# Kernel tuning notes

Hardware: AMD Instinct MI355X
Metric: run time of the kernel (lower is better)

The kernel has to match this reference:

```python
import jax, jax.numpy as jnp
import numpy as np

B, IC, H, W = 8, 16, 32, 32
OC, KH, KW = 32, 3, 3
PAD, K = 1, 2
OH, OW = H, W  # stride 1, pad 1, dilation 1 with 3x3 kernel
TABLES = OC * IC * KH * KW  # 4608, one LUT per (oc, ic, kh, kw)
M = TABLES * K              # 9216 mask rows
NUM_ENTRIES = 2 ** K


def setup_inputs() -> dict:
    key = jax.random.key(0)
    k1, k2, k3, k4, k5 = jax.random.split(key, 5)
    inp = jax.random.normal(k1, (B, IC, H, W), dtype=jnp.float32)
    w_luts = jax.random.normal(k2, (TABLES, NUM_ENTRIES), dtype=jnp.float32)
    mask_c = jax.random.randint(k3, (M,), 0, IC)
    mask_kh = jax.random.randint(k4, (M,), 0, KH)
    mask_kw = jax.random.randint(k5, (M,), 0, KW)
    return {"input": inp, "w_luts": w_luts, "mask_c": mask_c,
            "mask_kh": mask_kh, "mask_kw": mask_kw}


def _truth_table():
    # tt[j, i] in {-1, +1}: sign of bit j of truth-table entry i
    entries = jnp.arange(NUM_ENTRIES)
    bits = (entries[None, :] >> jnp.arange(K)[:, None]) & 1  # (K, 2^K)
    return (2 * bits - 1).astype(jnp.float32)


def reference(input, w_luts, mask_c, mask_kh, mask_kw):
    # Fused unfold (im2col) + per-table input_mask gather: instead of
    # materializing folded_input (B, L, IC, KH, KW), gather straight from the
    # padded image: expanded[b, oh, ow, m] = padded[b, c_m, oh + kh_m, ow + kw_m]
    padded = jnp.pad(input, ((0, 0), (0, 0), (PAD, PAD), (PAD, PAD)))
    row = jnp.arange(OH)[:, None] + mask_kh[None, :]   # (OH, M)
    col = jnp.arange(OW)[:, None] + mask_kw[None, :]   # (OW, M)
    expanded = padded[:, mask_c[None, None, :], row[:, None, :], col[None, :, :]]  # (B, OH, OW, M)

    # LagrangeTrainer: per-table soft LUT lookup via Lagrange interpolation
    x = expanded.reshape(B * OH * OW, TABLES, K)
    tt = _truth_table()                                       # (K, 2^K)
    factors = (1.0 + x[..., :, None] * tt[None, None]) * 0.5  # (N, T, K, 2^K)
    basis = jnp.prod(factors, axis=-2)                        # (N, T, 2^K)
    out = jnp.einsum('nte,te->nt', basis, w_luts)             # (N, TABLES)

    # Fold-style reshape + sum over the IC*KH*KW tables feeding each output
    out = out.reshape(B, OC, OH, OW, -1).sum(-1)
    out = out.reshape(B, OH * OW, OC).swapaxes(1, 2).reshape(B, OC, OH, OW)
    return out
```

## Files before the change

kernel.cpp:

```cpp
#include <hip/hip_runtime.h>

#define OC_ 32
#define IC_ 16
#define H_ 32
#define W_ 32
#define B_ 8
#define TPO 144

#define ROWS_PER_WG 16
#define TR 18
#define TC 34
#define CH_STRIDE (TR * TC)
#define TILE_F (IC_ * CH_STRIDE)

#define NQ 4
#define TQ (TPO / NQ)
#define NTHR 1024

struct alignas(16) Rec4 { unsigned offs; float bb, cc, dd; };

__global__ __launch_bounds__(NTHR, 8)
void conv_kernel(const float* __restrict__ input,
                 const float* __restrict__ w_luts,
                 const int*   __restrict__ mask_c,
                 const int*   __restrict__ mask_kh,
                 const int*   __restrict__ mask_kw,
                 float*       __restrict__ out) {
    __shared__ float tile[TILE_F];
    __shared__ Rec4  srec[TPO];
    __shared__ float sAA[TPO];
    __shared__ float sP[8];
    __shared__ float redA[NTHR];
    __shared__ float redB[NTHR];

    const int oh0 = blockIdx.x * ROWS_PER_WG;
    const int oc  = blockIdx.y;
    const int b   = blockIdx.z;
    const int tid = threadIdx.x;

    if (tid < TPO) {
        int t = oc * TPO + tid;
        const float4 w = *reinterpret_cast<const float4*>(w_luts + 4 * t);
        int m0 = 2 * t, m1 = m0 + 1;
        unsigned off0 = (unsigned)(mask_c[m0] * CH_STRIDE + mask_kh[m0] * TC + mask_kw[m0]) * 4u;
        unsigned off1 = (unsigned)(mask_c[m1] * CH_STRIDE + mask_kh[m1] * TC + mask_kw[m1]) * 4u;
        Rec4 r;
        r.offs = off0 | (off1 << 16);
        r.bb = 0.25f * (-w.x + w.y - w.z + w.w);
        r.cc = 0.25f * (-w.x - w.y + w.z + w.w);
        r.dd = 0.25f * ( w.x - w.y - w.z + w.w);
        srec[tid] = r;
        sAA[tid]  = 0.25f * (w.x + w.y + w.z + w.w);
    }

    const float* inb = input + b * (IC_ * H_ * W_);
    for (int u = tid; u < IC_ * TR * 8; u += NTHR) {
        int ch  = u / (TR * 8);
        int rem = u - ch * (TR * 8);
        int r   = rem >> 3;
        int c4  = (rem & 7) * 4;
        int grow = oh0 + r - 1;
        float4 v = make_float4(0.f, 0.f, 0.f, 0.f);
        if ((unsigned)grow < (unsigned)H_)
            v = *reinterpret_cast<const float4*>(inb + (ch * H_ + grow) * W_ + c4);
        float* dst = &tile[ch * CH_STRIDE + r * TC + 1 + c4];
        dst[0] = v.x; dst[1] = v.y; dst[2] = v.z; dst[3] = v.w;
    }
    for (int i = tid; i < IC_ * TR * 2; i += NTHR) {
        int ch  = i / (TR * 2);
        int rem = i - ch * (TR * 2);
        int r   = rem >> 1;
        int cc2 = (rem & 1) ? (TC - 1) : 0;
        tile[ch * CH_STRIDE + r * TC + cc2] = 0.f;
    }
    __syncthreads();

    if (tid < 8) {
        float s = 0.f;
        #pragma unroll
        for (int i = 0; i < 18; ++i) s += sAA[tid * 18 + i];
        sP[tid] = s;
    }

    const int pos = tid & 255;
    const int qt  = tid >> 8;
    const int rl  = pos >> 5;
    const int ow  = pos & 31;
    const char* tb = (const char*)tile + ((2 * rl) * TC + ow) * 4;
    const int4* sq = reinterpret_cast<const int4*>(srec);

    float accA = 0.f, accB = 0.f;
    const int t0 = qt * TQ;
    #pragma unroll 6
    for (int t = t0; t < t0 + TQ; ++t) {
        const int4 q = sq[t];
        const unsigned offs = (unsigned)q.x;
        const float* g0 = reinterpret_cast<const float*>(tb + (offs & 0xffffu));
        const float* g1 = reinterpret_cast<const float*>(tb + (offs >> 16));
        const float x0a = g0[0];
        const float x0b = g0[TC];
        const float x1a = g1[0];
        const float x1b = g1[TC];
        const float bb = __int_as_float(q.y);
        const float cc = __int_as_float(q.z);
        const float dd = __int_as_float(q.w);
        accA = fmaf(bb, x0a, accA);
        accA = fmaf(x1a, fmaf(dd, x0a, cc), accA);
        accB = fmaf(bb, x0b, accB);
        accB = fmaf(x1b, fmaf(dd, x0b, cc), accB);
    }
    redA[tid] = accA;
    redB[tid] = accB;
    __syncthreads();

    if (tid < 256) {
        const float bias = ((sP[0] + sP[1]) + (sP[2] + sP[3]))
                         + ((sP[4] + sP[5]) + (sP[6] + sP[7]));
        float a = (redA[tid] + redA[tid + 256]) + (redA[tid + 512] + redA[tid + 768]);
        float bsum = (redB[tid] + redB[tid + 256]) + (redB[tid + 512] + redB[tid + 768]);
        const int ohA = oh0 + 2 * rl;
        out[((b * OC_ + oc) * H_ + ohA    ) * W_ + ow] = a + bias;
        out[((b * OC_ + oc) * H_ + ohA + 1) * W_ + ow] = bsum + bias;
    }
}

extern "C" void kernel_launch(void* const* d_in, const int* in_sizes, int n_in,
                              void* d_out, int out_size, void* d_ws, size_t ws_size,
                              hipStream_t stream) {
    const float* input   = (const float*)d_in[0];
    const float* w_luts  = (const float*)d_in[1];
    const int*   mask_c  = (const int*)d_in[2];
    const int*   mask_kh = (const int*)d_in[3];
    const int*   mask_kw = (const int*)d_in[4];
    float* out = (float*)d_out;

    conv_kernel<<<dim3(H_ / ROWS_PER_WG, OC_, B_), dim3(NTHR), 0, stream>>>(
        input, w_luts, mask_c, mask_kh, mask_kw, out);
}
```

Before: 70.24 us.

## Process full image per workgroup with four output rows per thread

New measurement: 69.75 us. About the same (-0.7%).

```diff
diff --git a/kernel.cpp b/kernel.cpp
--- a/kernel.cpp
+++ b/kernel.cpp
@@ -7,10 +7,9 @@
 #define B_ 8
 #define TPO 144
 
-#define ROWS_PER_WG 16
-#define TR 18
+#define TRF 34
 #define TC 34
-#define CH_STRIDE (TR * TC)
+#define CH_STRIDE (TRF * TC)
 #define TILE_F (IC_ * CH_STRIDE)
 
 #define NQ 4
@@ -19,7 +18,7 @@
 
 struct alignas(16) Rec4 { unsigned offs; float bb, cc, dd; };
 
-__global__ __launch_bounds__(NTHR, 8)
+__global__ __launch_bounds__(NTHR, 1)
 void conv_kernel(const float* __restrict__ input,
                  const float* __restrict__ w_luts,
                  const int*   __restrict__ mask_c,
@@ -32,18 +31,19 @@
     __shared__ float sP[8];
     __shared__ float redA[NTHR];
     __shared__ float redB[NTHR];
+    __shared__ float redC[NTHR];
+    __shared__ float redD[NTHR];
 
-    const int oh0 = blockIdx.x * ROWS_PER_WG;
-    const int oc  = blockIdx.y;
-    const int b   = blockIdx.z;
+    const int oc  = blockIdx.x;
+    const int b   = blockIdx.y;
     const int tid = threadIdx.x;
 
     if (tid < TPO) {
         int t = oc * TPO + tid;
         const float4 w = *reinterpret_cast<const float4*>(w_luts + 4 * t);
         int m0 = 2 * t, m1 = m0 + 1;
-        unsigned off0 = (unsigned)(mask_c[m0] * CH_STRIDE + mask_kh[m0] * TC + mask_kw[m0]) * 4u;
-        unsigned off1 = (unsigned)(mask_c[m1] * CH_STRIDE + mask_kh[m1] * TC + mask_kw[m1]) * 4u;
+        unsigned off0 = (unsigned)(mask_c[m0] * CH_STRIDE + mask_kh[m0] * TC + mask_kw[m0]);
+        unsigned off1 = (unsigned)(mask_c[m1] * CH_STRIDE + mask_kh[m1] * TC + mask_kw[m1]);
         Rec4 r;
         r.offs = off0 | (off1 << 16);
         r.bb = 0.25f * (-w.x + w.y - w.z + w.w);
@@ -54,24 +54,28 @@
     }
 
     const float* inb = input + b * (IC_ * H_ * W_);
-    for (int u = tid; u < IC_ * TR * 8; u += NTHR) {
-        int ch  = u / (TR * 8);
-        int rem = u - ch * (TR * 8);
+    for (int u = tid; u < IC_ * H_ * 8; u += NTHR) {
+        int ch  = u >> 8;
+        int rem = u & 255;
         int r   = rem >> 3;
         int c4  = (rem & 7) * 4;
-        int grow = oh0 + r - 1;
-        float4 v = make_float4(0.f, 0.f, 0.f, 0.f);
-        if ((unsigned)grow < (unsigned)H_)
-            v = *reinterpret_cast<const float4*>(inb + (ch * H_ + grow) * W_ + c4);
-        float* dst = &tile[ch * CH_STRIDE + r * TC + 1 + c4];
+        const float4 v = *reinterpret_cast<const float4*>(inb + (ch * H_ + r) * W_ + c4);
+        float* dst = &tile[ch * CH_STRIDE + (r + 1) * TC + 1 + c4];
         dst[0] = v.x; dst[1] = v.y; dst[2] = v.z; dst[3] = v.w;
     }
-    for (int i = tid; i < IC_ * TR * 2; i += NTHR) {
-        int ch  = i / (TR * 2);
-        int rem = i - ch * (TR * 2);
+    for (int i = tid; i < IC_ * 2 * TC; i += NTHR) {
+        int ch  = i / (2 * TC);
+        int rem = i - ch * (2 * TC);
+        int row = (rem >= TC) ? (TRF - 1) : 0;
+        int col = (rem >= TC) ? (rem - TC) : rem;
+        tile[ch * CH_STRIDE + row * TC + col] = 0.f;
+    }
+    for (int i = tid; i < IC_ * TRF * 2; i += NTHR) {
+        int ch  = i / (TRF * 2);
+        int rem = i - ch * (TRF * 2);
         int r   = rem >> 1;
-        int cc2 = (rem & 1) ? (TC - 1) : 0;
-        tile[ch * CH_STRIDE + r * TC + cc2] = 0.f;
+        int col = (rem & 1) ? (TC - 1) : 0;
+        tile[ch * CH_STRIDE + r * TC + col] = 0.f;
     }
     __syncthreads();
 
@@ -82,45 +86,53 @@
         sP[tid] = s;
     }
 
-    const int pos = tid & 255;
-    const int qt  = tid >> 8;
-    const int rl  = pos >> 5;
-    const int ow  = pos & 31;
-    const char* tb = (const char*)tile + ((2 * rl) * TC + ow) * 4;
+    const int g  = tid >> 8;
+    const int p  = tid & 255;
+    const int rl = p >> 5;
+    const int ow = p & 31;
+    const float* tb = &tile[(4 * rl) * TC + ow];
     const int4* sq = reinterpret_cast<const int4*>(srec);
 
-    float accA = 0.f, accB = 0.f;
-    const int t0 = qt * TQ;
+    float a0 = 0.f, a1 = 0.f, a2 = 0.f, a3 = 0.f;
+    const int t0 = g * TQ;
     #pragma unroll 6
     for (int t = t0; t < t0 + TQ; ++t) {
         const int4 q = sq[t];
         const unsigned offs = (unsigned)q.x;
-        const float* g0 = reinterpret_cast<const float*>(tb + (offs & 0xffffu));
-        const float* g1 = reinterpret_cast<const float*>(tb + (offs >> 16));
-        const float x0a = g0[0];
-        const float x0b = g0[TC];
-        const float x1a = g1[0];
-        const float x1b = g1[TC];
+        const float* g0 = tb + (offs & 0xffffu);
+        const float* g1 = tb + (offs >> 16);
+        const float x00 = g0[0];
+        const float x01 = g0[TC];
+        const float x02 = g0[2 * TC];
+        const float x03 = g0[3 * TC];
+        const float x10 = g1[0];
+        const float x11 = g1[TC];
+        const float x12 = g1[2 * TC];
+        const float x13 = g1[3 * TC];
         const float bb = __int_as_float(q.y);
         const float cc = __int_as_float(q.z);
         const float dd = __int_as_float(q.w);
-        accA = fmaf(bb, x0a, accA);
-        accA = fmaf(x1a, fmaf(dd, x0a, cc), accA);
-        accB = fmaf(bb, x0b, accB);
-        accB = fmaf(x1b, fmaf(dd, x0b, cc), accB);
+        a0 = fmaf(bb, x00, a0);  a0 = fmaf(x10, fmaf(dd, x00, cc), a0);
+        a1 = fmaf(bb, x01, a1);  a1 = fmaf(x11, fmaf(dd, x01, cc), a1);
+        a2 = fmaf(bb, x02, a2);  a2 = fmaf(x12, fmaf(dd, x02, cc), a2);
+        a3 = fmaf(bb, x03, a3);  a3 = fmaf(x13, fmaf(dd, x03, cc), a3);
     }
-    redA[tid] = accA;
-    redB[tid] = accB;
+    redA[tid] = a0; redB[tid] = a1; redC[tid] = a2; redD[tid] = a3;
     __syncthreads();
 
     if (tid < 256) {
         const float bias = ((sP[0] + sP[1]) + (sP[2] + sP[3]))
                          + ((sP[4] + sP[5]) + (sP[6] + sP[7]));
-        float a = (redA[tid] + redA[tid + 256]) + (redA[tid + 512] + redA[tid + 768]);
-        float bsum = (redB[tid] + redB[tid + 256]) + (redB[tid + 512] + redB[tid + 768]);
-        const int ohA = oh0 + 2 * rl;
-        out[((b * OC_ + oc) * H_ + ohA    ) * W_ + ow] = a + bias;
-        out[((b * OC_ + oc) * H_ + ohA + 1) * W_ + ow] = bsum + bias;
+        float s0 = (redA[tid] + redA[tid + 256]) + (redA[tid + 512] + redA[tid + 768]);
+        float s1 = (redB[tid] + redB[tid + 256]) + (redB[tid + 512] + redB[tid + 768]);
+        float s2 = (redC[tid] + redC[tid + 256]) + (redC[tid + 512] + redC[tid + 768]);
+        float s3 = (redD[tid] + redD[tid + 256]) + (redD[tid + 512] + redD[tid + 768]);
+        const int y0 = 4 * rl;
+        float* ob = out + ((b * OC_ + oc) * H_ + y0) * W_ + ow;
+        ob[0 * W_] = s0 + bias;
+        ob[1 * W_] = s1 + bias;
+        ob[2 * W_] = s2 + bias;
+        ob[3 * W_] = s3 + bias;
     }
 }
 
@@ -134,6 +146,6 @@
     const int*   mask_kw = (const int*)d_in[4];
     float* out = (float*)d_out;
 
-    conv_kernel<<<dim3(H_ / ROWS_PER_WG, OC_, B_), dim3(NTHR), 0, stream>>>(
+    conv_kernel<<<dim3(OC_, B_), dim3(NTHR), 0, stream>>>(
         input, w_luts, mask_c, mask_kh, mask_kw, out);
 }
```
